# Performance work log

Hardware: AMD Instinct MI355X
Metric: run time of the kernel (lower is better)

## Reference

```python
import jax, jax.numpy as jnp
import numpy as np

BS, N, H = 16, 128, 256
L, F = 9, 48  # lat_embed_dim, frac_embed_dim = 6*frac_freq
IN_DIM = 2 * H + L + F


def setup_inputs() -> dict:
    key = jax.random.key(0)
    ks = jax.random.split(key, 7)
    node_embed = jax.random.normal(ks[0], (BS, N, H), dtype=jnp.float32)
    edge_embed = jax.random.normal(ks[1], (BS, N, N, F), dtype=jnp.float32)
    graph_embed = jax.random.normal(ks[2], (BS, L), dtype=jnp.float32)
    s1 = 1.0 / np.sqrt(IN_DIM)
    s2 = 1.0 / np.sqrt(H)
    W1 = jax.random.uniform(ks[3], (IN_DIM, H), jnp.float32, -s1, s1)
    b1 = jax.random.uniform(ks[4], (H,), jnp.float32, -s1, s1)
    W2 = jax.random.uniform(ks[5], (H, H), jnp.float32, -s2, s2)
    b2 = jax.random.uniform(ks[6], (H,), jnp.float32, -s2, s2)
    return {"node_embed": node_embed, "edge_embed": edge_embed,
            "graph_embed": graph_embed, "W1": W1, "b1": b1, "W2": W2, "b2": b2}


def reference(node_embed, edge_embed, graph_embed, W1, b1, W2, b2):
    bs, n, h = node_embed.shape
    # Concat order matches torch: [node_j, node_i, graph, edge_ij]
    # First linear is applied to the concat; split W1 by segment so we never
    # materialize the (bs, N, N, 2H+L+F) concat tensor (same math).
    Wj = W1[:h]            # acts on node_embed[b, j]
    Wi = W1[h:2 * h]       # acts on node_embed[b, i]
    Wg = W1[2 * h:2 * h + L]  # acts on graph_embed[b]
    We = W1[2 * h + L:]    # acts on edge_embed[b, i, j]
    pj = node_embed @ Wj                      # (bs, N, H) -> broadcast over i
    pi = node_embed @ Wi                      # (bs, N, H) -> broadcast over j
    pg = graph_embed @ Wg                     # (bs, H)
    pe = jnp.einsum('bijf,fh->bijh', edge_embed, We)  # (bs, N, N, H)
    z1 = pe + pj[:, None, :, :] + pi[:, :, None, :] + pg[:, None, None, :] + b1
    h1 = jax.nn.silu(z1)
    edge_msg = jax.nn.silu(h1 @ W2 + b2)      # (bs, N, N, H)
    node_msg = edge_msg.mean(axis=2)          # mean over j
    return node_msg
```

## Files before the change

### kernel.cpp

```cpp
#include <hip/hip_runtime.h>

#define BSZ 16
#define NN  128
#define HH  256
#define LLG 9
#define FFE 48

typedef float        f32x4 __attribute__((ext_vector_type(4)));
typedef _Float16     f16x8 __attribute__((ext_vector_type(8)));
typedef unsigned int u32x4 __attribute__((ext_vector_type(4)));

static __device__ __forceinline__ unsigned short f2h_bits(float x) {
    _Float16 h = (_Float16)x;
    return __builtin_bit_cast(unsigned short, h);
}

static __device__ __forceinline__ float fast_silu(float x) {
    float e = __builtin_amdgcn_exp2f(x * -1.44269504088896341f);
    return x * __builtin_amdgcn_rcpf(1.0f + e);
}

__global__ __launch_bounds__(256) void pre_w(
    const float* __restrict__ W1, const float* __restrict__ W2,
    unsigned short* __restrict__ W2T, unsigned short* __restrict__ WeT)
{
    int tid = blockIdx.x * 256 + threadIdx.x;
    {
        int ho = tid >> 8, k = tid & 255;
        W2T[(ho << 8) + k] = f2h_bits(W2[(k << 8) + ho]);
    }
    if (tid < 256 * 64) {
        int h = tid >> 6, f = tid & 63;
        WeT[(h << 6) + f] = (f < FFE) ? f2h_bits(W1[(521 + f) * HH + h])
                                      : (unsigned short)0;
    }
}

__global__ __launch_bounds__(256) void pre_pjbase(
    const float* __restrict__ node, const float* __restrict__ graph,
    const float* __restrict__ W1, const float* __restrict__ b1,
    float* __restrict__ pj, float* __restrict__ base)
{
    __shared__ float nrow[4][HH];
    __shared__ float gsh[LLG];
    const int blk = blockIdx.x;
    const int b = blk >> 5;
    const int r0 = (blk & 31) << 2;
    const int h = threadIdx.x;

    for (int t = h; t < 4 * HH; t += 256) {
        int r = t >> 8, k = t & 255;
        nrow[r][k] = node[(((size_t)b * NN) + r0 + r) * HH + k];
    }
    if (h < LLG) gsh[h] = graph[b * LLG + h];
    __syncthreads();

    float accj[4] = {0,0,0,0};
    float acci[4] = {0,0,0,0};
    for (int k = 0; k < HH; ++k) {
        float wj = W1[k * HH + h];
        float wi = W1[(k + HH) * HH + h];
        #pragma unroll
        for (int r = 0; r < 4; ++r) {
            float nv = nrow[r][k];
            accj[r] = fmaf(nv, wj, accj[r]);
            acci[r] = fmaf(nv, wi, acci[r]);
        }
    }
    float accg = b1[h];
    #pragma unroll
    for (int l = 0; l < LLG; ++l)
        accg = fmaf(gsh[l], W1[(2 * HH + l) * HH + h], accg);

    #pragma unroll
    for (int r = 0; r < 4; ++r) {
        size_t off = (((size_t)b * NN) + r0 + r) * HH + h;
        pj[off]   = accj[r];
        base[off] = acci[r] + accg;
    }
}

__global__ __launch_bounds__(512, 4) void fused_msg(
    const float* __restrict__ edge, const float* __restrict__ pj,
    const float* __restrict__ base, const unsigned short* __restrict__ W2T,
    const unsigned short* __restrict__ WeT, const float* __restrict__ b2,
    float* __restrict__ out)
{
    __shared__ unsigned char h1s[NN * HH * 2];
    __shared__ unsigned char efs[NN * 64 * 2];
    const int tid  = threadIdx.x;
    const int w    = tid >> 6;
    const int lane = tid & 63;
    const int q    = lane >> 4;
    const int c    = lane & 15;
    const int bi   = blockIdx.x;
    const int b    = bi >> 7;

    const float* eb = edge + (size_t)bi * (NN * FFE);

    #pragma unroll
    for (int p = 0; p < 3; ++p) {
        const int e4 = p * 512 + tid;
        const int j  = e4 / 12;
        const int f4 = e4 - j * 12;
        const f32x4 x = *reinterpret_cast<const f32x4*>(eb + (e4 << 2));
        unsigned int lo = __builtin_bit_cast(unsigned int,
                            __builtin_amdgcn_cvt_pkrtz(x[0], x[1]));
        unsigned int hi = __builtin_bit_cast(unsigned int,
                            __builtin_amdgcn_cvt_pkrtz(x[2], x[3]));
        const unsigned int off = (unsigned)(j << 7) +
            (((unsigned)(f4 << 3)) ^ ((unsigned)(j & 7) << 4));
        *reinterpret_cast<uint2*>(&efs[off]) = make_uint2(lo, hi);
    }
    {
        const int j = tid >> 2, g = tid & 3;
        const unsigned int off = (unsigned)(j << 7) +
            (((unsigned)(96 + (g << 3))) ^ ((unsigned)(j & 7) << 4));
        *reinterpret_cast<uint2*>(&efs[off]) = make_uint2(0u, 0u);
    }
    __syncthreads();

    f32x4 acc1[2][8];
    #pragma unroll
    for (int mt = 0; mt < 2; ++mt)
        #pragma unroll
        for (int nt = 0; nt < 8; ++nt) acc1[mt][nt] = f32x4{0.f, 0.f, 0.f, 0.f};

    #pragma unroll
    for (int kk = 0; kk < 2; ++kk) {
        const int koff = (kk << 5) + (q << 3);
        const int fb   = koff << 1;
        f16x8 af[2];
        #pragma unroll
        for (int mt = 0; mt < 2; ++mt) {
            const int row = (w << 5) + (mt << 4) + c;
            af[mt] = *reinterpret_cast<const f16x8*>(WeT + (row << 6) + koff);
        }
        #pragma unroll
        for (int nt = 0; nt < 8; ++nt) {
            const int j = (nt << 4) + c;
            const f16x8 bf = *reinterpret_cast<const f16x8*>(
                &efs[(unsigned)(j << 7) +
                     (((unsigned)fb) ^ ((unsigned)(j & 7) << 4))]);
            #pragma unroll
            for (int mt = 0; mt < 2; ++mt)
                acc1[mt][nt] = __builtin_amdgcn_mfma_f32_16x16x32_f16(
                    af[mt], bf, acc1[mt][nt], 0, 0, 0);
        }
    }

    #pragma unroll
    for (int mt = 0; mt < 2; ++mt) {
        const int h0 = (w << 5) + (mt << 4) + (q << 2);
        const f32x4 bb = *reinterpret_cast<const f32x4*>(
            base + ((size_t)bi << 8) + h0);
        #pragma unroll
        for (int nt = 0; nt < 8; ++nt) {
            const int jc = (nt << 4) + c;
            const f32x4 pjv = *reinterpret_cast<const f32x4*>(
                pj + (((size_t)b << 7) + jc) * HH + h0);
            float s0 = fast_silu(acc1[mt][nt][0] + bb[0] + pjv[0]);
            float s1 = fast_silu(acc1[mt][nt][1] + bb[1] + pjv[1]);
            float s2 = fast_silu(acc1[mt][nt][2] + bb[2] + pjv[2]);
            float s3 = fast_silu(acc1[mt][nt][3] + bb[3] + pjv[3]);
            unsigned int lo = __builtin_bit_cast(unsigned int,
                                __builtin_amdgcn_cvt_pkrtz(s0, s1));
            unsigned int hi = __builtin_bit_cast(unsigned int,
                                __builtin_amdgcn_cvt_pkrtz(s2, s3));
            const unsigned int off = (unsigned)(jc << 9) +
                (((unsigned)(h0 << 1)) ^ ((unsigned)(jc & 7) << 4));
            *reinterpret_cast<uint2*>(&h1s[off]) = make_uint2(lo, hi);
        }
    }
    __syncthreads();

    f32x4 acc2[8][2];
    #pragma unroll
    for (int mt = 0; mt < 8; ++mt)
        #pragma unroll
        for (int nt = 0; nt < 2; ++nt) acc2[mt][nt] = f32x4{0.f, 0.f, 0.f, 0.f};

    #pragma unroll 2
    for (int kk = 0; kk < 8; ++kk) {
        const int kb = (kk << 6) + (q << 4);
        f16x8 bw[2];
        #pragma unroll
        for (int nt = 0; nt < 2; ++nt) {
            const int ho = (w << 5) + (nt << 4) + c;
            bw[nt] = *reinterpret_cast<const f16x8*>(
                W2T + (ho << 8) + (kk << 5) + (q << 3));
        }
        #pragma unroll
        for (int g = 0; g < 2; ++g) {
            f16x8 a2[4];
            #pragma unroll
            for (int m = 0; m < 4; ++m) {
                const int jc = ((g << 2) + m) * 16 + c;
                const unsigned int off = (unsigned)(jc << 9) +
                    (((unsigned)kb) ^ ((unsigned)(jc & 7) << 4));
                a2[m] = *reinterpret_cast<const f16x8*>(&h1s[off]);
            }
            #pragma unroll
            for (int m = 0; m < 4; ++m)
                #pragma unroll
                for (int nt = 0; nt < 2; ++nt)
                    acc2[(g << 2) + m][nt] = __builtin_amdgcn_mfma_f32_16x16x32_f16(
                        a2[m], bw[nt], acc2[(g << 2) + m][nt], 0, 0, 0);
        }
    }

    float b2v[2];
    #pragma unroll
    for (int nt = 0; nt < 2; ++nt) b2v[nt] = b2[(w << 5) + (nt << 4) + c];

    float s[2] = {0.f, 0.f};
    #pragma unroll
    for (int nt = 0; nt < 2; ++nt)
        #pragma unroll
        for (int mt = 0; mt < 8; ++mt)
            #pragma unroll
            for (int r = 0; r < 4; ++r)
                s[nt] += fast_silu(acc2[mt][nt][r] + b2v[nt]);

    #pragma unroll
    for (int nt = 0; nt < 2; ++nt) {
        s[nt] += __shfl_xor(s[nt], 16);
        s[nt] += __shfl_xor(s[nt], 32);
    }
    if (q < 2)
        out[((size_t)bi << 8) + (w << 5) + (q << 4) + c] = s[q] * 0.0078125f;
}

extern "C" void kernel_launch(void* const* d_in, const int* in_sizes, int n_in,
                              void* d_out, int out_size, void* d_ws, size_t ws_size,
                              hipStream_t stream)
{
    const float* node  = (const float*)d_in[0];
    const float* edge  = (const float*)d_in[1];
    const float* graph = (const float*)d_in[2];
    const float* W1    = (const float*)d_in[3];
    const float* b1    = (const float*)d_in[4];
    const float* W2    = (const float*)d_in[5];
    const float* b2    = (const float*)d_in[6];
    float* out = (float*)d_out;

    char* ws = (char*)d_ws;
    unsigned short* W2T = (unsigned short*)ws;
    unsigned short* WeT = (unsigned short*)(ws + 131072);
    float* pj   = (float*)(ws + 163840);
    float* base = (float*)(ws + 163840 + 2097152);

    pre_w     <<<256, 256, 0, stream>>>(W1, W2, W2T, WeT);
    pre_pjbase<<<512, 256, 0, stream>>>(node, graph, W1, b1, pj, base);
    fused_msg <<<BSZ * NN, 512, 0, stream>>>(edge, pj, base, W2T, WeT, b2, out);
}
```

Baseline: 107.8 us.

## Process j dimension in two 64-row chunks with prefetch of next edge chunk

The fused kernel now handles the 128 j-columns in two chunks of 64, which halves the shared memory for the h1 and edge staging buffers. This should let more blocks be resident per CU. The global loads for the second edge chunk are issued before the first chunk's second GEMM, so their latency can overlap that compute. The cost is extra barriers, a second pass through the GEMM setup, and the mean accumulation now spanning both chunks.

```diff
diff --git a/kernel.cpp b/kernel.cpp
--- a/kernel.cpp
+++ b/kernel.cpp
@@ -5,6 +5,7 @@
 #define HH  256
 #define LLG 9
 #define FFE 48
+#define JC  64
 
 typedef float        f32x4 __attribute__((ext_vector_type(4)));
 typedef _Float16     f16x8 __attribute__((ext_vector_type(8)));
@@ -86,8 +87,8 @@
     const unsigned short* __restrict__ WeT, const float* __restrict__ b2,
     float* __restrict__ out)
 {
-    __shared__ unsigned char h1s[NN * HH * 2];
-    __shared__ unsigned char efs[NN * 64 * 2];
+    __shared__ unsigned char h1s[JC * HH * 2];
+    __shared__ unsigned char efs[JC * 64 * 2];
     const int tid  = threadIdx.x;
     const int w    = tid >> 6;
     const int lane = tid & 63;
@@ -98,12 +99,14 @@
 
     const float* eb = edge + (size_t)bi * (NN * FFE);
 
-    #pragma unroll
-    for (int p = 0; p < 3; ++p) {
-        const int e4 = p * 512 + tid;
+    float b2v[2];
+    #pragma unroll
+    for (int nt = 0; nt < 2; ++nt) b2v[nt] = b2[(w << 5) + (nt << 4) + c];
+    float s[2] = {0.f, 0.f};
+
+    auto stage_write = [&](f32x4 x, int e4) {
         const int j  = e4 / 12;
         const int f4 = e4 - j * 12;
-        const f32x4 x = *reinterpret_cast<const f32x4*>(eb + (e4 << 2));
         unsigned int lo = __builtin_bit_cast(unsigned int,
                             __builtin_amdgcn_cvt_pkrtz(x[0], x[1]));
         unsigned int hi = __builtin_bit_cast(unsigned int,
@@ -111,116 +114,139 @@
         const unsigned int off = (unsigned)(j << 7) +
             (((unsigned)(f4 << 3)) ^ ((unsigned)(j & 7) << 4));
         *reinterpret_cast<uint2*>(&efs[off]) = make_uint2(lo, hi);
-    }
-    {
+    };
+
+    if (tid < 256) {
         const int j = tid >> 2, g = tid & 3;
         const unsigned int off = (unsigned)(j << 7) +
             (((unsigned)(96 + (g << 3))) ^ ((unsigned)(j & 7) << 4));
         *reinterpret_cast<uint2*>(&efs[off]) = make_uint2(0u, 0u);
     }
-    __syncthreads();
-
-    f32x4 acc1[2][8];
-    #pragma unroll
-    for (int mt = 0; mt < 2; ++mt)
-        #pragma unroll
-        for (int nt = 0; nt < 8; ++nt) acc1[mt][nt] = f32x4{0.f, 0.f, 0.f, 0.f};
-
-    #pragma unroll
-    for (int kk = 0; kk < 2; ++kk) {
-        const int koff = (kk << 5) + (q << 3);
-        const int fb   = koff << 1;
-        f16x8 af[2];
+
+    {
+        f32x4 xa = *reinterpret_cast<const f32x4*>(eb + (tid << 2));
+        stage_write(xa, tid);
+        if (tid < 256) {
+            f32x4 xb = *reinterpret_cast<const f32x4*>(eb + ((512 + tid) << 2));
+            stage_write(xb, 512 + tid);
+        }
+    }
+    __syncthreads();
+
+    auto gemm1 = [&](int chunk) {
+        f32x4 acc1[2][4];
+        #pragma unroll
+        for (int mt = 0; mt < 2; ++mt)
+            #pragma unroll
+            for (int nt = 0; nt < 4; ++nt) acc1[mt][nt] = f32x4{0.f, 0.f, 0.f, 0.f};
+
+        #pragma unroll
+        for (int kk = 0; kk < 2; ++kk) {
+            const int koff = (kk << 5) + (q << 3);
+            const int fb   = koff << 1;
+            f16x8 af[2];
+            #pragma unroll
+            for (int mt = 0; mt < 2; ++mt) {
+                const int row = (w << 5) + (mt << 4) + c;
+                af[mt] = *reinterpret_cast<const f16x8*>(WeT + (row << 6) + koff);
+            }
+            #pragma unroll
+            for (int nt = 0; nt < 4; ++nt) {
+                const int j = (nt << 4) + c;
+                const f16x8 bf = *reinterpret_cast<const f16x8*>(
+                    &efs[(unsigned)(j << 7) +
+                         (((unsigned)fb) ^ ((unsigned)(j & 7) << 4))]);
+                #pragma unroll
+                for (int mt = 0; mt < 2; ++mt)
+                    acc1[mt][nt] = __builtin_amdgcn_mfma_f32_16x16x32_f16(
+                        af[mt], bf, acc1[mt][nt], 0, 0, 0);
+            }
+        }
+
         #pragma unroll
         for (int mt = 0; mt < 2; ++mt) {
-            const int row = (w << 5) + (mt << 4) + c;
-            af[mt] = *reinterpret_cast<const f16x8*>(WeT + (row << 6) + koff);
-        }
-        #pragma unroll
-        for (int nt = 0; nt < 8; ++nt) {
-            const int j = (nt << 4) + c;
-            const f16x8 bf = *reinterpret_cast<const f16x8*>(
-                &efs[(unsigned)(j << 7) +
-                     (((unsigned)fb) ^ ((unsigned)(j & 7) << 4))]);
-            #pragma unroll
-            for (int mt = 0; mt < 2; ++mt)
-                acc1[mt][nt] = __builtin_amdgcn_mfma_f32_16x16x32_f16(
-                    af[mt], bf, acc1[mt][nt], 0, 0, 0);
-        }
-    }
-
-    #pragma unroll
-    for (int mt = 0; mt < 2; ++mt) {
-        const int h0 = (w << 5) + (mt << 4) + (q << 2);
-        const f32x4 bb = *reinterpret_cast<const f32x4*>(
-            base + ((size_t)bi << 8) + h0);
-        #pragma unroll
-        for (int nt = 0; nt < 8; ++nt) {
-            const int jc = (nt << 4) + c;
-            const f32x4 pjv = *reinterpret_cast<const f32x4*>(
-                pj + (((size_t)b << 7) + jc) * HH + h0);
-            float s0 = fast_silu(acc1[mt][nt][0] + bb[0] + pjv[0]);
-            float s1 = fast_silu(acc1[mt][nt][1] + bb[1] + pjv[1]);
-            float s2 = fast_silu(acc1[mt][nt][2] + bb[2] + pjv[2]);
-            float s3 = fast_silu(acc1[mt][nt][3] + bb[3] + pjv[3]);
-            unsigned int lo = __builtin_bit_cast(unsigned int,
-                                __builtin_amdgcn_cvt_pkrtz(s0, s1));
-            unsigned int hi = __builtin_bit_cast(unsigned int,
-                                __builtin_amdgcn_cvt_pkrtz(s2, s3));
-            const unsigned int off = (unsigned)(jc << 9) +
-                (((unsigned)(h0 << 1)) ^ ((unsigned)(jc & 7) << 4));
-            *reinterpret_cast<uint2*>(&h1s[off]) = make_uint2(lo, hi);
-        }
-    }
-    __syncthreads();
-
-    f32x4 acc2[8][2];
-    #pragma unroll
-    for (int mt = 0; mt < 8; ++mt)
-        #pragma unroll
-        for (int nt = 0; nt < 2; ++nt) acc2[mt][nt] = f32x4{0.f, 0.f, 0.f, 0.f};
-
-    #pragma unroll 2
-    for (int kk = 0; kk < 8; ++kk) {
-        const int kb = (kk << 6) + (q << 4);
-        f16x8 bw[2];
-        #pragma unroll
-        for (int nt = 0; nt < 2; ++nt) {
-            const int ho = (w << 5) + (nt << 4) + c;
-            bw[nt] = *reinterpret_cast<const f16x8*>(
-                W2T + (ho << 8) + (kk << 5) + (q << 3));
-        }
-        #pragma unroll
-        for (int g = 0; g < 2; ++g) {
+            const int h0 = (w << 5) + (mt << 4) + (q << 2);
+            const f32x4 bb = *reinterpret_cast<const f32x4*>(
+                base + ((size_t)bi << 8) + h0);
+            #pragma unroll
+            for (int nt = 0; nt < 4; ++nt) {
+                const int jc = (nt << 4) + c;
+                const int jg = (chunk << 6) + jc;
+                const f32x4 pjv = *reinterpret_cast<const f32x4*>(
+                    pj + (((size_t)b << 7) + jg) * HH + h0);
+                float s0 = fast_silu(acc1[mt][nt][0] + bb[0] + pjv[0]);
+                float s1 = fast_silu(acc1[mt][nt][1] + bb[1] + pjv[1]);
+                float s2 = fast_silu(acc1[mt][nt][2] + bb[2] + pjv[2]);
+                float s3 = fast_silu(acc1[mt][nt][3] + bb[3] + pjv[3]);
+                unsigned int lo = __builtin_bit_cast(unsigned int,
+                                    __builtin_amdgcn_cvt_pkrtz(s0, s1));
+                unsigned int hi = __builtin_bit_cast(unsigned int,
+                                    __builtin_amdgcn_cvt_pkrtz(s2, s3));
+                const unsigned int off = (unsigned)(jc << 9) +
+                    (((unsigned)(h0 << 1)) ^ ((unsigned)(jc & 7) << 4));
+                *reinterpret_cast<uint2*>(&h1s[off]) = make_uint2(lo, hi);
+            }
+        }
+    };
+
+    auto gemm2 = [&]() {
+        f32x4 acc2[4][2];
+        #pragma unroll
+        for (int m = 0; m < 4; ++m)
+            #pragma unroll
+            for (int nt = 0; nt < 2; ++nt) acc2[m][nt] = f32x4{0.f, 0.f, 0.f, 0.f};
+
+        const unsigned short* wp0 = W2T + (((w << 5) + c) << 8) + (q << 3);
+        const unsigned short* wp1 = wp0 + (16 << 8);
+
+        #pragma unroll 2
+        for (int kk = 0; kk < 8; ++kk) {
+            const f16x8 bw0 = *reinterpret_cast<const f16x8*>(wp0 + (kk << 5));
+            const f16x8 bw1 = *reinterpret_cast<const f16x8*>(wp1 + (kk << 5));
+            const int kb = (kk << 6) + (q << 4);
             f16x8 a2[4];
             #pragma unroll
             for (int m = 0; m < 4; ++m) {
-                const int jc = ((g << 2) + m) * 16 + c;
+                const int jc = (m << 4) + c;
                 const unsigned int off = (unsigned)(jc << 9) +
                     (((unsigned)kb) ^ ((unsigned)(jc & 7) << 4));
                 a2[m] = *reinterpret_cast<const f16x8*>(&h1s[off]);
             }
             #pragma unroll
+            for (int m = 0; m < 4; ++m) {
+                acc2[m][0] = __builtin_amdgcn_mfma_f32_16x16x32_f16(
+                    a2[m], bw0, acc2[m][0], 0, 0, 0);
+                acc2[m][1] = __builtin_amdgcn_mfma_f32_16x16x32_f16(
+                    a2[m], bw1, acc2[m][1], 0, 0, 0);
+            }
+        }
+
+        #pragma unroll
+        for (int nt = 0; nt < 2; ++nt)
+            #pragma unroll
             for (int m = 0; m < 4; ++m)
                 #pragma unroll
-                for (int nt = 0; nt < 2; ++nt)
-                    acc2[(g << 2) + m][nt] = __builtin_amdgcn_mfma_f32_16x16x32_f16(
-                        a2[m], bw[nt], acc2[(g << 2) + m][nt], 0, 0, 0);
-        }
-    }
-
-    float b2v[2];
-    #pragma unroll
-    for (int nt = 0; nt < 2; ++nt) b2v[nt] = b2[(w << 5) + (nt << 4) + c];
-
-    float s[2] = {0.f, 0.f};
-    #pragma unroll
-    for (int nt = 0; nt < 2; ++nt)
-        #pragma unroll
-        for (int mt = 0; mt < 8; ++mt)
-            #pragma unroll
-            for (int r = 0; r < 4; ++r)
-                s[nt] += fast_silu(acc2[mt][nt][r] + b2v[nt]);
+                for (int r = 0; r < 4; ++r)
+                    s[nt] += fast_silu(acc2[m][nt][r] + b2v[nt]);
+    };
+
+    gemm1(0);
+    __syncthreads();
+
+    f32x4 xa = *reinterpret_cast<const f32x4*>(eb + 3072 + (tid << 2));
+    f32x4 xb = {0.f, 0.f, 0.f, 0.f};
+    if (tid < 256)
+        xb = *reinterpret_cast<const f32x4*>(eb + 3072 + ((512 + tid) << 2));
+
+    gemm2();
+
+    stage_write(xa, tid);
+    if (tid < 256) stage_write(xb, 512 + tid);
+    __syncthreads();
+
+    gemm1(1);
+    __syncthreads();
+    gemm2();
 
     #pragma unroll
     for (int nt = 0; nt < 2; ++nt) {
```

New measurement: 142.6 us. +32.4%, slower.
